# Performance work log

Measured on AMD Instinct MI355X. Metric: run time of the kernel, lower is better.

## Reference

```python
import jax, jax.numpy as jnp
import numpy as np

B, S, T, N, D, L = 8192, 10, 3, 65536, 128, 2  # batch, neigh len, node types, table size, embed_d, layers
NEG_SLOPE = 0.01  # torch LeakyReLU default


def setup_inputs() -> dict:
    key = jax.random.key(0)
    ks = jax.random.split(key, 6)
    return {
        "emb": jax.random.normal(ks[0], (T, N, D), jnp.float32) * 0.02,
        "Wih": jax.random.normal(ks[1], (L, T, D, D), jnp.float32) / np.sqrt(D).astype(np.float32),
        "Whh": jax.random.normal(ks[2], (L, T, D, D), jnp.float32) / np.sqrt(D).astype(np.float32),
        "bih": jnp.full((L, T, D), 0.1, jnp.float32),
        "bhh": jnp.full((L, T, D), 0.1, jnp.float32),
        "w_att": jax.random.normal(ks[3], (L, 2 * D), jnp.float32) / np.sqrt(2 * D).astype(np.float32),
        "ids": jax.random.randint(ks[4], (B,), 0, N),
        "neigh_idx": jax.random.randint(ks[5], (T, B, S), 0, N),
    }


def _rnn_mean(x, Wih_l, Whh_l, bih_l, bhh_l):
    """x: [T,B,S,D] neighbor embeds. torch nn.RNN(tanh): h_s = tanh(x_s@Wih^T + bih + h@Whh^T + bhh).
    Returns mean of all hidden states over time: [T,B,D]."""
    xs = jnp.moveaxis(x, 2, 0)  # [S, T, B, D]
    h0 = jnp.zeros((T, B, D), x.dtype)

    def step(h, x_s):
        h = jnp.tanh(jnp.einsum('tbd,ted->tbe', x_s, Wih_l) + bih_l[:, None, :]
                     + jnp.einsum('tbd,ted->tbe', h, Whh_l) + bhh_l[:, None, :])
        return h, h

    _, hs = jax.lax.scan(step, h0, xs)  # [S, T, B, D]
    return hs.mean(axis=0)


def reference(emb, Wih, Whh, bih, bhh, w_att, ids, neigh_idx):
    cur = emb[0][ids]  # [B, D] target node type = 0
    # per-type neighbor gather from base embedding tables (same each layer, as in source)
    neigh = jax.vmap(lambda e, i: e[i])(emb, neigh_idx)  # [T, B, S, D]
    for l in range(L):
        agg = _rnn_mean(neigh, Wih[l], Whh[l], bih[l], bhh[l])  # [T, B, D]
        cands = jnp.moveaxis(jnp.concatenate([cur[None], agg], axis=0), 0, 1)  # [B, 1+T, D]
        feat = jnp.concatenate(
            [jnp.broadcast_to(cur[:, None, :], cands.shape), cands], axis=-1)  # [B, 1+T, 2D]
        scores = feat @ w_att[l]  # [B, 1+T]
        w = jax.nn.softmax(scores, axis=1)[..., None]
        cur = jax.nn.leaky_relu(jnp.sum(w * cands, axis=1), NEG_SLOPE)
    return cur
```

## Files before the change

kernel.cpp:

```cpp
#include <hip/hip_runtime.h>
#include <hip/hip_bf16.h>

#define NB   8192
#define NS   10
#define NT   3
#define NN   65536
#define ND   128
#define NL   2
#define ROWS 32

typedef __attribute__((ext_vector_type(8))) short bf16x8;
typedef __attribute__((ext_vector_type(4))) float f32x4;

__device__ __forceinline__ unsigned int pk2(float lo, float hi) {
    unsigned int r;
    asm("v_cvt_pk_bf16_f32 %0, %1, %2" : "=v"(r) : "v"(lo), "v"(hi));
    return r;
}
__device__ __forceinline__ float tanh_f(float x) {
    float e, r;
    asm("v_exp_f32 %0, %1" : "=v"(e) : "v"(x * 2.88539004f));
    asm("v_rcp_f32 %0, %1" : "=v"(r) : "v"(e + 1.0f));
    return fmaf(-2.0f, r, 1.0f);
}
__device__ __forceinline__ void bar_lgkm() {
    asm volatile("s_waitcnt lgkmcnt(0)\n\ts_barrier" ::: "memory");
}

__global__ __launch_bounds__(512)
void rnn_kernel(const float* __restrict__ emb, const float* __restrict__ Wih,
                const float* __restrict__ Whh, const float* __restrict__ bih,
                const float* __restrict__ bhh, const int* __restrict__ nidx,
                float* __restrict__ agg)
{
    __shared__ __align__(16) char lds[6 * 8192];

    const int bid = blockIdx.x;
    const int t   = bid / (NB / ROWS);
    const int b0  = (bid % (NB / ROWS)) * ROWS;

    const int tid  = threadIdx.x;
    const int wv   = tid >> 6;
    const int lay  = wv >> 2;
    const int lane = tid & 63;
    const int l16  = lane & 15;
    const int lg   = lane >> 4;
    const int e0   = (wv & 3) * 32;
    const int rx   = l16 & 7;

    char* xb = lds;
    char* hb = lds + 16384 + lay * 16384;

    const int srow  = tid >> 4;
    const int sq    = tid & 15;
    const int xaddr = srow * 256 + ((sq ^ (srow & 7)) << 4);

    const int* ip = nidx + ((size_t)t * NB + b0 + srow) * NS;
    int idxs[NS];
    #pragma unroll
    for (int s = 0; s < NS; ++s) idxs[s] = ip[s];

    float4 P0, P1;
    {
        const float* src = emb + ((size_t)t * NN + idxs[0]) * ND + sq * 8;
        P0 = *(const float4*)(src);
        P1 = *(const float4*)(src + 4);
    }

    const float* Wih_lt = Wih + (size_t)(lay * NT + t) * ND * ND;
    const float* Whh_lt = Whh + (size_t)(lay * NT + t) * ND * ND;
    const float* bih_lt = bih + (size_t)(lay * NT + t) * ND;
    const float* bhh_lt = bhh + (size_t)(lay * NT + t) * ND;

    bf16x8 Af[2][8];
    #pragma unroll
    for (int mt = 0; mt < 2; ++mt) {
        #pragma unroll
        for (int kc = 0; kc < 8; ++kc) {
            const float* Wsrc = (kc < 4) ? Wih_lt : Whh_lt;
            const float* srcp = Wsrc + (size_t)(e0 + mt * 16 + l16) * ND + (kc & 3) * 32 + lg * 8;
            float4 p0 = *(const float4*)(srcp);
            float4 p1 = *(const float4*)(srcp + 4);
            int4 a;
            a.x = (int)pk2(p0.x, p0.y);
            a.y = (int)pk2(p0.z, p0.w);
            a.z = (int)pk2(p1.x, p1.y);
            a.w = (int)pk2(p1.z, p1.w);
            Af[mt][kc] = *(bf16x8*)&a;
        }
    }

    f32x4 biasv[2];
    #pragma unroll
    for (int mt = 0; mt < 2; ++mt)
        #pragma unroll
        for (int i = 0; i < 4; ++i) {
            int e = e0 + mt * 16 + lg * 4 + i;
            biasv[mt][i] = bih_lt[e] + bhh_lt[e];
        }

    int raddr[2][4];
    #pragma unroll
    for (int nt = 0; nt < 2; ++nt)
        #pragma unroll
        for (int c = 0; c < 4; ++c)
            raddr[nt][c] = (nt * 16 + l16) * 256 + (((c * 4 + lg) ^ rx) << 4);
    int hwaddr[2][2];
    #pragma unroll
    for (int nt = 0; nt < 2; ++nt)
        #pragma unroll
        for (int mt = 0; mt < 2; ++mt) {
            int es = e0 + mt * 16 + lg * 4;
            hwaddr[nt][mt] = (nt * 16 + l16) * 256 + (((es >> 3) ^ rx) << 4) + (es & 7) * 2;
        }

    f32x4 zero4; zero4[0] = 0.f; zero4[1] = 0.f; zero4[2] = 0.f; zero4[3] = 0.f;
    f32x4 Ag[2][2];
    #pragma unroll
    for (int nt = 0; nt < 2; ++nt) { Ag[nt][0] = zero4; Ag[nt][1] = zero4; }

    #pragma unroll
    for (int s = 0; s < NS; ++s) {
        {
            int4 pk;
            pk.x = (int)pk2(P0.x, P0.y);
            pk.y = (int)pk2(P0.z, P0.w);
            pk.z = (int)pk2(P1.x, P1.y);
            pk.w = (int)pk2(P1.z, P1.w);
            *(int4*)(xb + xaddr + (s & 1) * 8192) = pk;
        }
        if (s + 1 < NS) {
            const float* src = emb + ((size_t)t * NN + idxs[s + 1]) * ND + sq * 8;
            P0 = *(const float4*)(src);
            P1 = *(const float4*)(src + 4);
        }
        bar_lgkm();

        f32x4 acc[2][2];
        #pragma unroll
        for (int nt = 0; nt < 2; ++nt) { acc[nt][0] = biasv[0]; acc[nt][1] = biasv[1]; }

        #pragma unroll
        for (int nt = 0; nt < 2; ++nt)
            #pragma unroll
            for (int c = 0; c < 4; ++c) {
                bf16x8 bf = *(const bf16x8*)(xb + raddr[nt][c] + (s & 1) * 8192);
                acc[nt][0] = __builtin_amdgcn_mfma_f32_16x16x32_bf16(Af[0][c], bf, acc[nt][0], 0, 0, 0);
                acc[nt][1] = __builtin_amdgcn_mfma_f32_16x16x32_bf16(Af[1][c], bf, acc[nt][1], 0, 0, 0);
            }
        if (s > 0) {
            #pragma unroll
            for (int nt = 0; nt < 2; ++nt)
                #pragma unroll
                for (int c = 0; c < 4; ++c) {
                    bf16x8 bf = *(const bf16x8*)(hb + raddr[nt][c] + ((s + 1) & 1) * 8192);
                    acc[nt][0] = __builtin_amdgcn_mfma_f32_16x16x32_bf16(Af[0][c + 4], bf, acc[nt][0], 0, 0, 0);
                    acc[nt][1] = __builtin_amdgcn_mfma_f32_16x16x32_bf16(Af[1][c + 4], bf, acc[nt][1], 0, 0, 0);
                }
        }

        #pragma unroll
        for (int nt = 0; nt < 2; ++nt)
            #pragma unroll
            for (int mt = 0; mt < 2; ++mt) {
                f32x4 h;
                #pragma unroll
                for (int i = 0; i < 4; ++i)
                    h[i] = tanh_f(acc[nt][mt][i]);
                Ag[nt][mt] += h;
                int2 pk;
                pk.x = (int)pk2(h[0], h[1]);
                pk.y = (int)pk2(h[2], h[3]);
                *(int2*)(hb + hwaddr[nt][mt] + (s & 1) * 8192) = pk;
            }
    }

    float* aggp = agg + ((size_t)(lay * NT + t) * NB + b0) * ND;
    #pragma unroll
    for (int nt = 0; nt < 2; ++nt) {
        int b = nt * 16 + l16;
        #pragma unroll
        for (int mt = 0; mt < 2; ++mt) {
            f32x4 v = Ag[nt][mt] * 0.1f;
            *(f32x4*)(aggp + (size_t)b * ND + e0 + mt * 16 + lg * 4) = v;
        }
    }
}

__global__ __launch_bounds__(256)
void att_kernel(const float* __restrict__ emb, const int* __restrict__ ids,
                const float* __restrict__ w_att, const float* __restrict__ agg,
                float* __restrict__ cur, const int l)
{
    const int wid  = threadIdx.x >> 6;
    const int lane = threadIdx.x & 63;
    const int b    = blockIdx.x * 4 + wid;

    const float* waH  = w_att + l * 2 * ND;
    const float* waT  = waH + ND;
    const float* crow = (l == 0) ? (emb + (size_t)ids[b] * ND) : (cur + (size_t)b * ND);
    const float* ab   = agg + ((size_t)(l * NT) * NB + b) * ND;

    const float c1 = crow[lane], c2 = crow[lane + 64];
    const float h1 = waH[lane],  h2 = waH[lane + 64];
    const float t1 = waT[lane],  t2 = waT[lane + 64];
    float g1[3], g2[3];
    #pragma unroll
    for (int tt = 0; tt < 3; ++tt) {
        g1[tt] = ab[(size_t)tt * NB * ND + lane];
        g2[tt] = ab[(size_t)tt * NB * ND + lane + 64];
    }

    float dH = c1 * h1 + c2 * h2;
    float dc = c1 * t1 + c2 * t2;
    float d0 = g1[0] * t1 + g2[0] * t2;
    float d1 = g1[1] * t1 + g2[1] * t2;
    float d2 = g1[2] * t1 + g2[2] * t2;
    #pragma unroll
    for (int off = 32; off > 0; off >>= 1) {
        dH += __shfl_xor(dH, off);
        dc += __shfl_xor(dc, off);
        d0 += __shfl_xor(d0, off);
        d1 += __shfl_xor(d1, off);
        d2 += __shfl_xor(d2, off);
    }

    float s0 = dH + dc, s1 = dH + d0, s2 = dH + d1, s3 = dH + d2;
    float m  = fmaxf(fmaxf(s0, s1), fmaxf(s2, s3));
    float q0 = __expf(s0 - m), q1 = __expf(s1 - m), q2 = __expf(s2 - m), q3 = __expf(s3 - m);
    float inv = __fdividef(1.0f, q0 + q1 + q2 + q3);
    float w0 = q0 * inv, w1 = q1 * inv, w2 = q2 * inv, w3 = q3 * inv;

    float o1 = w0 * c1 + w1 * g1[0] + w2 * g1[1] + w3 * g1[2];
    float o2 = w0 * c2 + w1 * g2[0] + w2 * g2[1] + w3 * g2[2];
    o1 = (o1 > 0.f) ? o1 : 0.01f * o1;
    o2 = (o2 > 0.f) ? o2 : 0.01f * o2;

    float* orow = cur + (size_t)b * ND;
    orow[lane]      = o1;
    orow[lane + 64] = o2;
}

extern "C" void kernel_launch(void* const* d_in, const int* in_sizes, int n_in,
                              void* d_out, int out_size, void* d_ws, size_t ws_size,
                              hipStream_t stream)
{
    const float* emb  = (const float*)d_in[0];
    const float* Wih  = (const float*)d_in[1];
    const float* Whh  = (const float*)d_in[2];
    const float* bih  = (const float*)d_in[3];
    const float* bhh  = (const float*)d_in[4];
    const float* watt = (const float*)d_in[5];
    const int*   ids  = (const int*)d_in[6];
    const int*   nidx = (const int*)d_in[7];

    float* cur = (float*)d_out;
    float* agg = (float*)d_ws;

    rnn_kernel<<<dim3(NT * (NB / ROWS)), dim3(512), 0, stream>>>(emb, Wih, Whh, bih, bhh, nidx, agg);
    att_kernel<<<dim3(NB / 4), dim3(256), 0, stream>>>(emb, ids, watt, agg, cur, 0);
    att_kernel<<<dim3(NB / 4), dim3(256), 0, stream>>>(emb, ids, watt, agg, cur, 1);
}
```

Baseline: 76.20 us.

## Halve RNN block rows, widen per-wave output tile to four M-tiles

Each RNN block now handles 16 batch rows with 256 threads (4 waves, 2 per layer) instead of 32 rows with 512 threads. Each wave covers 64 output features across four 16-wide M tiles and one N tile, so each B fragment read from LDS feeds four MFMAs. The bias load is vectorised. This doubles the grid and halves LDS per block to improve occupancy and cut LDS traffic, at the cost of more weight registers per wave (32 bf16x8 A fragments) and twice as many redundant weight loads and conversions across blocks.

```diff
diff --git a/kernel.cpp b/kernel.cpp
--- a/kernel.cpp
+++ b/kernel.cpp
@@ -7,7 +7,7 @@
 #define NN   65536
 #define ND   128
 #define NL   2
-#define ROWS 32
+#define ROWS 16
 
 typedef __attribute__((ext_vector_type(8))) short bf16x8;
 typedef __attribute__((ext_vector_type(4))) float f32x4;
@@ -27,13 +27,13 @@
     asm volatile("s_waitcnt lgkmcnt(0)\n\ts_barrier" ::: "memory");
 }
 
-__global__ __launch_bounds__(512)
+__global__ __launch_bounds__(256, 2)
 void rnn_kernel(const float* __restrict__ emb, const float* __restrict__ Wih,
                 const float* __restrict__ Whh, const float* __restrict__ bih,
                 const float* __restrict__ bhh, const int* __restrict__ nidx,
                 float* __restrict__ agg)
 {
-    __shared__ __align__(16) char lds[6 * 8192];
+    __shared__ __align__(16) char lds[6 * 4096];
 
     const int bid = blockIdx.x;
     const int t   = bid / (NB / ROWS);
@@ -41,15 +41,15 @@
 
     const int tid  = threadIdx.x;
     const int wv   = tid >> 6;
-    const int lay  = wv >> 2;
+    const int lay  = wv >> 1;
     const int lane = tid & 63;
     const int l16  = lane & 15;
     const int lg   = lane >> 4;
-    const int e0   = (wv & 3) * 32;
+    const int e0   = (wv & 1) * 64;
     const int rx   = l16 & 7;
 
     char* xb = lds;
-    char* hb = lds + 16384 + lay * 16384;
+    char* hb = lds + 8192 + lay * 8192;
 
     const int srow  = tid >> 4;
     const int sq    = tid & 15;
@@ -72,9 +72,9 @@
     const float* bih_lt = bih + (size_t)(lay * NT + t) * ND;
     const float* bhh_lt = bhh + (size_t)(lay * NT + t) * ND;
 
-    bf16x8 Af[2][8];
-    #pragma unroll
-    for (int mt = 0; mt < 2; ++mt) {
+    bf16x8 Af[4][8];
+    #pragma unroll
+    for (int mt = 0; mt < 4; ++mt) {
         #pragma unroll
         for (int kc = 0; kc < 8; ++kc) {
             const float* Wsrc = (kc < 4) ? Wih_lt : Whh_lt;
@@ -90,34 +90,33 @@
         }
     }
 
-    f32x4 biasv[2];
-    #pragma unroll
-    for (int mt = 0; mt < 2; ++mt)
-        #pragma unroll
-        for (int i = 0; i < 4; ++i) {
-            int e = e0 + mt * 16 + lg * 4 + i;
-            biasv[mt][i] = bih_lt[e] + bhh_lt[e];
-        }
-
-    int raddr[2][4];
-    #pragma unroll
-    for (int nt = 0; nt < 2; ++nt)
-        #pragma unroll
-        for (int c = 0; c < 4; ++c)
-            raddr[nt][c] = (nt * 16 + l16) * 256 + (((c * 4 + lg) ^ rx) << 4);
-    int hwaddr[2][2];
-    #pragma unroll
-    for (int nt = 0; nt < 2; ++nt)
-        #pragma unroll
-        for (int mt = 0; mt < 2; ++mt) {
-            int es = e0 + mt * 16 + lg * 4;
-            hwaddr[nt][mt] = (nt * 16 + l16) * 256 + (((es >> 3) ^ rx) << 4) + (es & 7) * 2;
-        }
+    f32x4 biasv[4];
+    #pragma unroll
+    for (int mt = 0; mt < 4; ++mt) {
+        int e = e0 + mt * 16 + lg * 4;
+        float4 bi = *(const float4*)(bih_lt + e);
+        float4 bh = *(const float4*)(bhh_lt + e);
+        biasv[mt][0] = bi.x + bh.x;
+        biasv[mt][1] = bi.y + bh.y;
+        biasv[mt][2] = bi.z + bh.z;
+        biasv[mt][3] = bi.w + bh.w;
+    }
+
+    int raddr[4];
+    #pragma unroll
+    for (int c = 0; c < 4; ++c)
+        raddr[c] = l16 * 256 + (((c * 4 + lg) ^ rx) << 4);
+    int hwaddr[4];
+    #pragma unroll
+    for (int mt = 0; mt < 4; ++mt) {
+        int es = e0 + mt * 16 + lg * 4;
+        hwaddr[mt] = l16 * 256 + (((es >> 3) ^ rx) << 4) + (es & 7) * 2;
+    }
 
     f32x4 zero4; zero4[0] = 0.f; zero4[1] = 0.f; zero4[2] = 0.f; zero4[3] = 0.f;
-    f32x4 Ag[2][2];
-    #pragma unroll
-    for (int nt = 0; nt < 2; ++nt) { Ag[nt][0] = zero4; Ag[nt][1] = zero4; }
+    f32x4 Ag[4];
+    #pragma unroll
+    for (int mt = 0; mt < 4; ++mt) Ag[mt] = zero4;
 
     #pragma unroll
     for (int s = 0; s < NS; ++s) {
@@ -127,7 +126,7 @@
             pk.y = (int)pk2(P0.z, P0.w);
             pk.z = (int)pk2(P1.x, P1.y);
             pk.w = (int)pk2(P1.z, P1.w);
-            *(int4*)(xb + xaddr + (s & 1) * 8192) = pk;
+            *(int4*)(xb + xaddr + (s & 1) * 4096) = pk;
         }
         if (s + 1 < NS) {
             const float* src = emb + ((size_t)t * NN + idxs[s + 1]) * ND + sq * 8;
@@ -136,54 +135,46 @@
         }
         bar_lgkm();
 
-        f32x4 acc[2][2];
-        #pragma unroll
-        for (int nt = 0; nt < 2; ++nt) { acc[nt][0] = biasv[0]; acc[nt][1] = biasv[1]; }
-
-        #pragma unroll
-        for (int nt = 0; nt < 2; ++nt)
+        f32x4 acc[4];
+        #pragma unroll
+        for (int mt = 0; mt < 4; ++mt) acc[mt] = biasv[mt];
+
+        #pragma unroll
+        for (int c = 0; c < 4; ++c) {
+            bf16x8 bf = *(const bf16x8*)(xb + raddr[c] + (s & 1) * 4096);
+            #pragma unroll
+            for (int mt = 0; mt < 4; ++mt)
+                acc[mt] = __builtin_amdgcn_mfma_f32_16x16x32_bf16(Af[mt][c], bf, acc[mt], 0, 0, 0);
+        }
+        if (s > 0) {
             #pragma unroll
             for (int c = 0; c < 4; ++c) {
-                bf16x8 bf = *(const bf16x8*)(xb + raddr[nt][c] + (s & 1) * 8192);
-                acc[nt][0] = __builtin_amdgcn_mfma_f32_16x16x32_bf16(Af[0][c], bf, acc[nt][0], 0, 0, 0);
-                acc[nt][1] = __builtin_amdgcn_mfma_f32_16x16x32_bf16(Af[1][c], bf, acc[nt][1], 0, 0, 0);
+                bf16x8 bf = *(const bf16x8*)(hb + raddr[c] + ((s + 1) & 1) * 4096);
+                #pragma unroll
+                for (int mt = 0; mt < 4; ++mt)
+                    acc[mt] = __builtin_amdgcn_mfma_f32_16x16x32_bf16(Af[mt][c + 4], bf, acc[mt], 0, 0, 0);
             }
-        if (s > 0) {
+        }
+
+        #pragma unroll
+        for (int mt = 0; mt < 4; ++mt) {
+            f32x4 h;
             #pragma unroll
-            for (int nt = 0; nt < 2; ++nt)
-                #pragma unroll
-                for (int c = 0; c < 4; ++c) {
-                    bf16x8 bf = *(const bf16x8*)(hb + raddr[nt][c] + ((s + 1) & 1) * 8192);
-                    acc[nt][0] = __builtin_amdgcn_mfma_f32_16x16x32_bf16(Af[0][c + 4], bf, acc[nt][0], 0, 0, 0);
-                    acc[nt][1] = __builtin_amdgcn_mfma_f32_16x16x32_bf16(Af[1][c + 4], bf, acc[nt][1], 0, 0, 0);
-                }
-        }
-
-        #pragma unroll
-        for (int nt = 0; nt < 2; ++nt)
-            #pragma unroll
-            for (int mt = 0; mt < 2; ++mt) {
-                f32x4 h;
-                #pragma unroll
-                for (int i = 0; i < 4; ++i)
-                    h[i] = tanh_f(acc[nt][mt][i]);
-                Ag[nt][mt] += h;
-                int2 pk;
-                pk.x = (int)pk2(h[0], h[1]);
-                pk.y = (int)pk2(h[2], h[3]);
-                *(int2*)(hb + hwaddr[nt][mt] + (s & 1) * 8192) = pk;
-            }
+            for (int i = 0; i < 4; ++i)
+                h[i] = tanh_f(acc[mt][i]);
+            Ag[mt] += h;
+            int2 pk;
+            pk.x = (int)pk2(h[0], h[1]);
+            pk.y = (int)pk2(h[2], h[3]);
+            *(int2*)(hb + hwaddr[mt] + (s & 1) * 4096) = pk;
+        }
     }
 
     float* aggp = agg + ((size_t)(lay * NT + t) * NB + b0) * ND;
     #pragma unroll
-    for (int nt = 0; nt < 2; ++nt) {
-        int b = nt * 16 + l16;
-        #pragma unroll
-        for (int mt = 0; mt < 2; ++mt) {
-            f32x4 v = Ag[nt][mt] * 0.1f;
-            *(f32x4*)(aggp + (size_t)b * ND + e0 + mt * 16 + lg * 4) = v;
-        }
+    for (int mt = 0; mt < 4; ++mt) {
+        f32x4 v = Ag[mt] * 0.1f;
+        *(f32x4*)(aggp + (size_t)l16 * ND + e0 + mt * 16 + lg * 4) = v;
     }
 }
 
@@ -257,7 +248,7 @@
     float* cur = (float*)d_out;
     float* agg = (float*)d_ws;
 
-    rnn_kernel<<<dim3(NT * (NB / ROWS)), dim3(512), 0, stream>>>(emb, Wih, Whh, bih, bhh, nidx, agg);
+    rnn_kernel<<<dim3(NT * (NB / ROWS)), dim3(256), 0, stream>>>(emb, Wih, Whh, bih, bhh, nidx, agg);
     att_kernel<<<dim3(NB / 4), dim3(256), 0, stream>>>(emb, ids, watt, agg, cur, 0);
     att_kernel<<<dim3(NB / 4), dim3(256), 0, stream>>>(emb, ids, watt, agg, cur, 1);
 }
```

New measurement: 138.5 us. 1.82x slower.
